# Performance work log

Hardware: AMD Instinct MI355X
Metric: run time of the kernel (lower is better)

Reference implementation:

```python
import jax, jax.numpy as jnp
import numpy as np

DIM = 4096
NUM_EXPERTS = 8
TOP_K = 2
TOKENS = 8192  # batch 2 * seq 4096


def setup_inputs() -> dict:
    key = jax.random.key(0)
    k1, k2 = jax.random.split(key)
    x = jax.random.normal(k1, (TOKENS, DIM), dtype=jnp.float32)
    W = jax.random.normal(k2, (NUM_EXPERTS, DIM), dtype=jnp.float32) * 0.02  # router weight, trunc-normal-ish
    return {"x": x, "W": W}


def reference(x, W):
    # Routing: linear -> top-k -> softmax over the k selected scores (fp32) -> cast back
    expert_scores = jnp.einsum("td,ed->te", x, W)                       # [T, E]
    top_scores, selected = jax.lax.top_k(expert_scores, TOP_K)          # [T, K], [T, K]
    top_scores = jax.nn.softmax(top_scores.astype(jnp.float32), axis=-1).astype(x.dtype)

    flat_expert_indices = selected.reshape(-1)                           # [T*K]
    # torch.histc(bins=E, min=0, max=E) on integer expert ids == bincount
    num_tokens_per_expert = jnp.bincount(flat_expert_indices, length=NUM_EXPERTS)

    # Stable argsort groups tokens by destination expert, preserving token order within an expert
    sorted_indices = jnp.argsort(flat_expert_indices, stable=True)       # [T*K]
    scatter_indices = sorted_indices // TOP_K                            # original token id per slot
    x_gathered = x[scatter_indices]                                      # [T*K, D]
    scores_sorted = top_scores.reshape(-1)[sorted_indices]               # [T*K]
    return x_gathered, num_tokens_per_expert, scatter_indices, scores_sorted
```

## Files before the change

kernel.cpp:

```cpp
#include <hip/hip_runtime.h>
#include <hip/hip_bf16.h>
#include <cstdint>

#define TOKENS 8192
#define DIM 4096
#define D4 (DIM / 4)
#define NEXP 8
#define TOPK 2
#define SLOTS (TOKENS * TOPK)
#define NCHUNK (SLOTS / 64)

#define OUT_CNT ((size_t)TOKENS * TOPK * DIM)
#define OUT_SCAT (OUT_CNT + NEXP)
#define OUT_SCORE (OUT_SCAT + SLOTS)

typedef float vfloat4 __attribute__((ext_vector_type(4)));

__global__ __launch_bounds__(256) void k_score(const float* __restrict__ x,
                                               const float* __restrict__ W,
                                               int* __restrict__ eid,
                                               float* __restrict__ prob)
{
    const int wave = threadIdx.x >> 6;
    const int lane = threadIdx.x & 63;
    const int tok0 = (blockIdx.x * 4 + wave) * 4;

    const float4* x4 = reinterpret_cast<const float4*>(x);
    const float4* W4 = reinterpret_cast<const float4*>(W);

    float acc[4][NEXP];
#pragma unroll
    for (int t = 0; t < 4; ++t)
#pragma unroll
        for (int e = 0; e < NEXP; ++e) acc[t][e] = 0.f;

    for (int i = 0; i < 16; ++i) {
        const int d4 = lane + 64 * i;
        float4 xv[4];
#pragma unroll
        for (int t = 0; t < 4; ++t) xv[t] = x4[(size_t)(tok0 + t) * D4 + d4];
#pragma unroll
        for (int e = 0; e < NEXP; ++e) {
            const float4 w = W4[e * D4 + d4];
#pragma unroll
            for (int t = 0; t < 4; ++t) {
                acc[t][e] = fmaf(xv[t].x, w.x, acc[t][e]);
                acc[t][e] = fmaf(xv[t].y, w.y, acc[t][e]);
                acc[t][e] = fmaf(xv[t].z, w.z, acc[t][e]);
                acc[t][e] = fmaf(xv[t].w, w.w, acc[t][e]);
            }
        }
    }

#pragma unroll
    for (int t = 0; t < 4; ++t)
#pragma unroll
        for (int e = 0; e < NEXP; ++e) {
            float v = acc[t][e];
#pragma unroll
            for (int off = 32; off >= 1; off >>= 1) v += __shfl_xor(v, off);
            acc[t][e] = v;
        }

#pragma unroll
    for (int t = 0; t < 4; ++t) {
        int i0 = 0;
        float m0 = acc[t][0];
#pragma unroll
        for (int e = 1; e < NEXP; ++e)
            if (acc[t][e] > m0) { m0 = acc[t][e]; i0 = e; }
        int i1 = -1;
        float m1 = -INFINITY;
#pragma unroll
        for (int e = 0; e < NEXP; ++e)
            if (e != i0 && acc[t][e] > m1) { m1 = acc[t][e]; i1 = e; }
        const float z = __expf(m1 - m0);
        const float inv = 1.0f / (1.0f + z);
        if (lane == t) {
            const int s2 = (tok0 + t) * 2;
            eid[s2] = i0;
            eid[s2 + 1] = i1;
            prob[s2] = inv;
            prob[s2 + 1] = z * inv;
        }
    }
}

__global__ __launch_bounds__(64) void k_hist(const int* __restrict__ eid,
                                             int* __restrict__ hist)
{
    const int c = blockIdx.x;
    const int lane = threadIdx.x;
    const int e = eid[c * 64 + lane];
#pragma unroll
    for (int q = 0; q < NEXP; ++q) {
        const unsigned long long m = __ballot(e == q);
        if (lane == q) hist[c * NEXP + q] = __popcll(m);
    }
}

__global__ __launch_bounds__(64) void k_scan(int* __restrict__ hist,
                                             float* __restrict__ out)
{
    const int lane = threadIdx.x;
    int run[NEXP];
#pragma unroll
    for (int q = 0; q < NEXP; ++q) run[q] = 0;

    int excl[4][NEXP];
    for (int r = 0; r < 4; ++r) {
        const int c = r * 64 + lane;
#pragma unroll
        for (int q = 0; q < NEXP; ++q) {
            const int v = hist[c * NEXP + q];
            int incl = v;
#pragma unroll
            for (int off = 1; off <= 32; off <<= 1) {
                const int n = __shfl_up(incl, off);
                if (lane >= off) incl += n;
            }
            excl[r][q] = run[q] + incl - v;
            run[q] += __shfl(incl, 63);
        }
    }
    int eoff[NEXP];
    int a = 0;
#pragma unroll
    for (int q = 0; q < NEXP; ++q) { eoff[q] = a; a += run[q]; }
    for (int r = 0; r < 4; ++r) {
        const int c = r * 64 + lane;
#pragma unroll
        for (int q = 0; q < NEXP; ++q) hist[c * NEXP + q] = excl[r][q] + eoff[q];
    }
    if (lane == 0) {
#pragma unroll
        for (int q = 0; q < NEXP; ++q) out[OUT_CNT + q] = (float)run[q];
    }
}

__global__ __launch_bounds__(64) void k_pos(const int* __restrict__ eid,
                                            const float* __restrict__ prob,
                                            const int* __restrict__ hist,
                                            int* __restrict__ dstpos,
                                            float* __restrict__ out)
{
    const int c = blockIdx.x;
    const int lane = threadIdx.x;
    const int s = c * 64 + lane;
    const int e = eid[s];
    const unsigned long long lt = (1ull << lane) - 1ull;
    int rank = 0;
#pragma unroll
    for (int q = 0; q < NEXP; ++q) {
        const unsigned long long m = __ballot(e == q);
        if (e == q) rank = __popcll(m & lt);
    }
    const int p = hist[c * NEXP + e] + rank;
    dstpos[s] = p;
    out[OUT_SCAT + p] = (float)(s >> 1);
    out[OUT_SCORE + p] = prob[s];
}

__global__ __launch_bounds__(256) void k_gather(const float* __restrict__ x,
                                                const int* __restrict__ dstpos,
                                                float* __restrict__ out)
{
    const int t = blockIdx.x;
    const int p0 = dstpos[t * 2];
    const int p1 = dstpos[t * 2 + 1];
    const vfloat4* x4 = reinterpret_cast<const vfloat4*>(x) + (size_t)t * D4;
    vfloat4* o4 = reinterpret_cast<vfloat4*>(out);
#pragma unroll
    for (int i = 0; i < 4; ++i) {
        const int idx = threadIdx.x + 256 * i;
        const vfloat4 v = x4[idx];
        __builtin_nontemporal_store(v, &o4[(size_t)p0 * D4 + idx]);
        __builtin_nontemporal_store(v, &o4[(size_t)p1 * D4 + idx]);
    }
}

extern "C" void kernel_launch(void* const* d_in, const int* in_sizes, int n_in,
                              void* d_out, int out_size, void* d_ws, size_t ws_size,
                              hipStream_t stream)
{
    const float* x = (const float*)d_in[0];
    const float* W = (const float*)d_in[1];
    float* out = (float*)d_out;

    int* eid = (int*)d_ws;
    float* prob = (float*)((char*)d_ws + 64 * 1024);
    int* dstpos = (int*)((char*)d_ws + 128 * 1024);
    int* hist = (int*)((char*)d_ws + 192 * 1024);

    k_score<<<TOKENS / 16, 256, 0, stream>>>(x, W, eid, prob);
    k_hist<<<NCHUNK, 64, 0, stream>>>(eid, hist);
    k_scan<<<1, 64, 0, stream>>>(hist, out);
    k_pos<<<NCHUNK, 64, 0, stream>>>(eid, prob, hist, dstpos, out);
    k_gather<<<TOKENS, 256, 0, stream>>>(x, dstpos, out);
}
```

Before: 390.0 us.

## Fuse routing, scan, and gather into one persistent kernel with grid barriers

Merges the five launches (score, hist, scan, pos, gather) into a single kernel of 512 blocks. Each block computes the top-2 routing for its 16 tokens, keeps the results in shared memory, and builds its histogram with shared atomics. Block 0 runs the global exclusive scan after an atomic grid barrier, and a second barrier publishes the offsets before each block gathers its own tokens while they may still sit in cache. This removes launch gaps and the global-memory round trips for eid, prob and dstpos. In exchange it relies on all 512 blocks being resident at once, which can deadlock if they are not, and it serializes on a single block doing the scan.

```diff
diff --git a/kernel.cpp b/kernel.cpp
--- a/kernel.cpp
+++ b/kernel.cpp
@@ -1,5 +1,4 @@
 #include <hip/hip_runtime.h>
-#include <hip/hip_bf16.h>
 #include <cstdint>
 
 #define TOKENS 8192
@@ -8,22 +7,36 @@
 #define NEXP 8
 #define TOPK 2
 #define SLOTS (TOKENS * TOPK)
-#define NCHUNK (SLOTS / 64)
-
-#define OUT_CNT ((size_t)TOKENS * TOPK * DIM)
+
+#define NBLK 512
+#define TPB 256
+#define TOK_PER_BLK 16
+#define CH 32
+
+#define OUT_CNT ((size_t)SLOTS * DIM)
 #define OUT_SCAT (OUT_CNT + NEXP)
 #define OUT_SCORE (OUT_SCAT + SLOTS)
 
 typedef float vfloat4 __attribute__((ext_vector_type(4)));
 
-__global__ __launch_bounds__(256) void k_score(const float* __restrict__ x,
-                                               const float* __restrict__ W,
-                                               int* __restrict__ eid,
-                                               float* __restrict__ prob)
+__global__ __launch_bounds__(TPB, 2) void k_moe(const float* __restrict__ x,
+                                                const float* __restrict__ W,
+                                                int* __restrict__ hist,
+                                                int* __restrict__ bar,
+                                                float* __restrict__ out)
 {
+    __shared__ int   s_eid[CH];
+    __shared__ float s_prob[CH];
+    __shared__ int   s_cnt[NEXP];
+    __shared__ int   s_pos[CH];
+
     const int wave = threadIdx.x >> 6;
     const int lane = threadIdx.x & 63;
-    const int tok0 = (blockIdx.x * 4 + wave) * 4;
+    const int blk  = blockIdx.x;
+    const int tok0 = (blk * 4 + wave) * 4;
+
+    if (threadIdx.x < NEXP) s_cnt[threadIdx.x] = 0;
+    __syncthreads();
 
     const float4* x4 = reinterpret_cast<const float4*>(x);
     const float4* W4 = reinterpret_cast<const float4*>(W);
@@ -77,105 +90,102 @@
         const float z = __expf(m1 - m0);
         const float inv = 1.0f / (1.0f + z);
         if (lane == t) {
-            const int s2 = (tok0 + t) * 2;
-            eid[s2] = i0;
-            eid[s2 + 1] = i1;
-            prob[s2] = inv;
-            prob[s2 + 1] = z * inv;
-        }
-    }
-}
-
-__global__ __launch_bounds__(64) void k_hist(const int* __restrict__ eid,
-                                             int* __restrict__ hist)
-{
-    const int c = blockIdx.x;
-    const int lane = threadIdx.x;
-    const int e = eid[c * 64 + lane];
-#pragma unroll
-    for (int q = 0; q < NEXP; ++q) {
-        const unsigned long long m = __ballot(e == q);
-        if (lane == q) hist[c * NEXP + q] = __popcll(m);
-    }
-}
-
-__global__ __launch_bounds__(64) void k_scan(int* __restrict__ hist,
-                                             float* __restrict__ out)
-{
-    const int lane = threadIdx.x;
-    int run[NEXP];
-#pragma unroll
-    for (int q = 0; q < NEXP; ++q) run[q] = 0;
-
-    int excl[4][NEXP];
-    for (int r = 0; r < 4; ++r) {
-        const int c = r * 64 + lane;
+            const int ls = (wave * 4 + t) * 2;
+            s_eid[ls]      = i0;
+            s_eid[ls + 1]  = i1;
+            s_prob[ls]     = inv;
+            s_prob[ls + 1] = z * inv;
+            atomicAdd(&s_cnt[i0], 1);
+            atomicAdd(&s_cnt[i1], 1);
+        }
+    }
+    __syncthreads();
+    if (threadIdx.x < NEXP) hist[blk * NEXP + threadIdx.x] = s_cnt[threadIdx.x];
+
+    __syncthreads();
+    if (threadIdx.x == 0) { __threadfence(); atomicAdd(&bar[0], 1); }
+
+    if (blk == 0) {
+        if (threadIdx.x == 0) {
+            while (__hip_atomic_load(&bar[0], __ATOMIC_ACQUIRE,
+                                     __HIP_MEMORY_SCOPE_AGENT) < NBLK)
+                __builtin_amdgcn_s_sleep(2);
+        }
+        __syncthreads();
+        if (threadIdx.x < 64) {
+            int v[NEXP][8];
+#pragma unroll
+            for (int q = 0; q < NEXP; ++q)
+#pragma unroll
+                for (int r = 0; r < 8; ++r)
+                    v[q][r] = hist[(r * 64 + lane) * NEXP + q];
+            int base = 0;
+#pragma unroll
+            for (int q = 0; q < NEXP; ++q) {
+                int run = 0;
+#pragma unroll
+                for (int r = 0; r < 8; ++r) {
+                    int incl = v[q][r];
+#pragma unroll
+                    for (int off = 1; off <= 32; off <<= 1) {
+                        const int n = __shfl_up(incl, off);
+                        if (lane >= off) incl += n;
+                    }
+                    hist[(r * 64 + lane) * NEXP + q] = base + run + incl - v[q][r];
+                    run += __shfl(incl, 63);
+                }
+                if (lane == 0) out[OUT_CNT + q] = (float)run;
+                base += run;
+            }
+        }
+    }
+
+    __syncthreads();
+    if (threadIdx.x == 0) {
+        __threadfence();
+        atomicAdd(&bar[32], 1);
+        while (__hip_atomic_load(&bar[32], __ATOMIC_ACQUIRE,
+                                 __HIP_MEMORY_SCOPE_AGENT) < NBLK)
+            __builtin_amdgcn_s_sleep(2);
+    }
+    __syncthreads();
+
+    if (threadIdx.x < 64) {
+        const int e = (lane < CH) ? s_eid[lane] : -1;
+        const unsigned long long lt = (1ull << lane) - 1ull;
+        int rank = 0;
 #pragma unroll
         for (int q = 0; q < NEXP; ++q) {
-            const int v = hist[c * NEXP + q];
-            int incl = v;
-#pragma unroll
-            for (int off = 1; off <= 32; off <<= 1) {
-                const int n = __shfl_up(incl, off);
-                if (lane >= off) incl += n;
-            }
-            excl[r][q] = run[q] + incl - v;
-            run[q] += __shfl(incl, 63);
-        }
-    }
-    int eoff[NEXP];
-    int a = 0;
-#pragma unroll
-    for (int q = 0; q < NEXP; ++q) { eoff[q] = a; a += run[q]; }
-    for (int r = 0; r < 4; ++r) {
-        const int c = r * 64 + lane;
-#pragma unroll
-        for (int q = 0; q < NEXP; ++q) hist[c * NEXP + q] = excl[r][q] + eoff[q];
-    }
-    if (lane == 0) {
-#pragma unroll
-        for (int q = 0; q < NEXP; ++q) out[OUT_CNT + q] = (float)run[q];
-    }
-}
-
-__global__ __launch_bounds__(64) void k_pos(const int* __restrict__ eid,
-                                            const float* __restrict__ prob,
-                                            const int* __restrict__ hist,
-                                            int* __restrict__ dstpos,
-                                            float* __restrict__ out)
-{
-    const int c = blockIdx.x;
-    const int lane = threadIdx.x;
-    const int s = c * 64 + lane;
-    const int e = eid[s];
-    const unsigned long long lt = (1ull << lane) - 1ull;
-    int rank = 0;
-#pragma unroll
-    for (int q = 0; q < NEXP; ++q) {
-        const unsigned long long m = __ballot(e == q);
-        if (e == q) rank = __popcll(m & lt);
-    }
-    const int p = hist[c * NEXP + e] + rank;
-    dstpos[s] = p;
-    out[OUT_SCAT + p] = (float)(s >> 1);
-    out[OUT_SCORE + p] = prob[s];
-}
-
-__global__ __launch_bounds__(256) void k_gather(const float* __restrict__ x,
-                                                const int* __restrict__ dstpos,
-                                                float* __restrict__ out)
-{
-    const int t = blockIdx.x;
-    const int p0 = dstpos[t * 2];
-    const int p1 = dstpos[t * 2 + 1];
-    const vfloat4* x4 = reinterpret_cast<const vfloat4*>(x) + (size_t)t * D4;
+            const unsigned long long m = __ballot(e == q);
+            if (e == q) rank = __popcll(m & lt);
+        }
+        if (lane < CH) {
+            const int p = hist[blk * NEXP + e] + rank;
+            s_pos[lane] = p;
+            const int s = blk * CH + lane;
+            out[OUT_SCAT + p]  = (float)(s >> 1);
+            out[OUT_SCORE + p] = s_prob[lane];
+        }
+    }
+    __syncthreads();
+
+    const vfloat4* xx = reinterpret_cast<const vfloat4*>(x) +
+                        (size_t)(blk * TOK_PER_BLK) * D4;
     vfloat4* o4 = reinterpret_cast<vfloat4*>(out);
-#pragma unroll
-    for (int i = 0; i < 4; ++i) {
-        const int idx = threadIdx.x + 256 * i;
-        const vfloat4 v = x4[idx];
-        __builtin_nontemporal_store(v, &o4[(size_t)p0 * D4 + idx]);
-        __builtin_nontemporal_store(v, &o4[(size_t)p1 * D4 + idx]);
+#pragma unroll 2
+    for (int tt = 0; tt < TOK_PER_BLK; ++tt) {
+        const int p0 = s_pos[2 * tt];
+        const int p1 = s_pos[2 * tt + 1];
+        const vfloat4* src = xx + (size_t)tt * D4;
+        vfloat4* d0 = o4 + (size_t)p0 * D4;
+        vfloat4* d1 = o4 + (size_t)p1 * D4;
+#pragma unroll
+        for (int i = 0; i < 4; ++i) {
+            const int idx = threadIdx.x + TPB * i;
+            const vfloat4 v = src[idx];
+            __builtin_nontemporal_store(v, d0 + idx);
+            __builtin_nontemporal_store(v, d1 + idx);
+        }
     }
 }
 
@@ -187,14 +197,9 @@
     const float* W = (const float*)d_in[1];
     float* out = (float*)d_out;
 
-    int* eid = (int*)d_ws;
-    float* prob = (float*)((char*)d_ws + 64 * 1024);
-    int* dstpos = (int*)((char*)d_ws + 128 * 1024);
-    int* hist = (int*)((char*)d_ws + 192 * 1024);
-
-    k_score<<<TOKENS / 16, 256, 0, stream>>>(x, W, eid, prob);
-    k_hist<<<NCHUNK, 64, 0, stream>>>(eid, hist);
-    k_scan<<<1, 64, 0, stream>>>(hist, out);
-    k_pos<<<NCHUNK, 64, 0, stream>>>(eid, prob, hist, dstpos, out);
-    k_gather<<<TOKENS, 256, 0, stream>>>(x, dstpos, out);
+    int* hist = (int*)d_ws;
+    int* bar  = (int*)((char*)d_ws + 64 * 1024);
+
+    hipMemsetAsync(bar, 0, 256, stream);
+    k_moe<<<NBLK, TPB, 0, stream>>>(x, W, hist, bar, out);
 }
```

Result: slower. 444.3 us (+13.9%).
